# Kernel tuning notes

Hardware: AMD Instinct MI355X
Metric: run time of the kernel (lower is better)

Reference implementation:

```python
import jax, jax.numpy as jnp
import numpy as np
from jax import lax

PAD_ID = 50256
POOL = 2  # maxout pool size


def setup_inputs() -> dict:
    key = jax.random.key(0)
    ks = jax.random.split(key, 20)
    B, T, S = 32, 64, 400
    V, DW, DM, DE, DK = 50257, 512, 512, 512, 64
    s = 0.02
    return {
        "tgt_seq": jax.random.randint(ks[0], (B, T), 0, V, dtype=jnp.int32),
        "src_seq": jax.random.randint(ks[1], (B, S), 0, V, dtype=jnp.int32),
        "enc_output": jax.random.normal(ks[2], (B, S, DE), dtype=jnp.float32),
        "hidden": jax.random.normal(ks[3], (B, DE), dtype=jnp.float32),
        "word_emb": jax.random.normal(ks[4], (V, DW), dtype=jnp.float32) * s,
        "W_init": jax.random.normal(ks[5], (DE, DM), dtype=jnp.float32) * s,
        "b_init": jnp.zeros((DM,), jnp.float32),
        "Wx": jax.random.normal(ks[6], (DW + DE, 3 * DM), dtype=jnp.float32) * s,
        "Wh": jax.random.normal(ks[7], (DM, 3 * DM), dtype=jnp.float32) * s,
        "bx": jnp.zeros((3 * DM,), jnp.float32),
        "bh": jnp.zeros((3 * DM,), jnp.float32),
        "Wc": jax.random.normal(ks[8], (DE, DK), dtype=jnp.float32) * s,
        "Wq": jax.random.normal(ks[9], (DM, DK), dtype=jnp.float32) * s,
        "w_cov": jax.random.normal(ks[10], (DK,), dtype=jnp.float32) * s,
        "v_att": jax.random.normal(ks[11], (DK,), dtype=jnp.float32) * s,
        "W_copy": jax.random.normal(ks[12], (DE + DM, 1), dtype=jnp.float32) * s,
        "b_copy": jnp.zeros((1,), jnp.float32),
        "W_read": jax.random.normal(ks[13], (DW + DM + DE, DM), dtype=jnp.float32) * s,
        "b_read": jnp.zeros((DM,), jnp.float32),
    }


def _gru_cell(x, h, Wx, Wh, bx, bh):
    gx = x @ Wx + bx
    gh = h @ Wh + bh
    rx, zx, nx = jnp.split(gx, 3, axis=-1)
    rh, zh, nh = jnp.split(gh, 3, axis=-1)
    r = jax.nn.sigmoid(rx + rh)
    z = jax.nn.sigmoid(zx + zh)
    n = jnp.tanh(nx + r * nh)
    return (1.0 - z) * n + z * h


def reference(tgt_seq, src_seq, enc_output, hidden, word_emb, W_init, b_init,
              Wx, Wh, bx, bh, Wc, Wq, w_cov, v_att, W_copy, b_copy, W_read, b_read):
    B, S, DE = enc_output.shape
    T = tgt_seq.shape[1]
    DM = Wh.shape[0]
    dt = enc_output.dtype

    pad_mask = (src_seq == PAD_ID)                       # [B,S]
    h0 = jnp.tanh(hidden @ W_init + b_init)              # DecInit  [B,DM]
    ctx0 = jnp.zeros((B, DE), dt)                        # attn_init
    cov0 = jnp.zeros((B, S), dt)
    precompute = jnp.einsum('bsd,dk->bsk', enc_output, Wc)  # computed once
    emb = jnp.swapaxes(word_emb[tgt_seq], 0, 1)          # [T,B,DW]

    def step(carry, x):
        h, ctx, cov = carry
        e, t = x
        rnn_in = jnp.concatenate([e, ctx], axis=1)       # input feed
        h = _gru_cell(rnn_in, h, Wx, Wh, bx, bh)
        # concat attention with coverage
        energy = jnp.tanh(precompute + (h @ Wq)[:, None, :]
                          + cov[:, :, None] * w_cov)     # [B,S,DK]
        scores = energy @ v_att                          # [B,S]
        scores = jnp.where(pad_mask, jnp.asarray(-1e9, dt), scores)
        attn = jax.nn.softmax(scores, axis=1)
        new_ctx = jnp.einsum('bs,bsd->bd', attn, enc_output)
        avg_cov = cov / jnp.maximum(t, 1).astype(dt)
        cov_loss = jnp.sum(jnp.minimum(attn, avg_cov), axis=1)
        next_cov = cov + attn
        copy_gate = jax.nn.sigmoid(jnp.concatenate([h, new_ctx], 1) @ W_copy + b_copy)
        readout = jnp.concatenate([e, h, new_ctx], 1) @ W_read + b_read
        maxo = readout.reshape(B, DM // POOL, POOL).max(axis=2)
        return (h, new_ctx, next_cov), (maxo, attn, copy_gate, cov_loss)

    (_, ctx_f, _), (pred, attns, gates, cov_losses) = lax.scan(
        step, (h0, ctx0, cov0), (emb, jnp.arange(T)))
    pred = jnp.swapaxes(pred, 0, 1)              # [B,T,DM//POOL]
    copy_pred = jnp.swapaxes(attns, 0, 1)        # [B,T,S]
    copy_gate = jnp.swapaxes(gates, 0, 1)        # [B,T,1]
    coverage_pred = jnp.swapaxes(cov_losses, 0, 1)  # [B,T]
    return (pred, attns[-1], ctx_f, copy_pred, copy_gate, coverage_pred)
```

## Files before the change

kernel.cpp:

```cpp
#include <hip/hip_runtime.h>
#include <cstdint>
#include <cstddef>


#define PAD_ID_C 50256

typedef float f32x4 __attribute__((ext_vector_type(4)));
typedef short bf16x8 __attribute__((ext_vector_type(8)));

__device__ __forceinline__ unsigned short f2bf(float x){
  union { float f; unsigned u; } v; v.f = x;
  unsigned r = (v.u + 0x7FFFu + ((v.u >> 16) & 1u)) >> 16;
  return (unsigned short)r;
}
__device__ __forceinline__ float bf2f(unsigned short h){
  union { unsigned u; float f; } v; v.u = ((unsigned)h) << 16; return v.f;
}
__device__ __forceinline__ float sigm_(float x){ return 1.f/(1.f+__expf(-x)); }
__device__ __forceinline__ float tanh_(float x){ float e=__expf(2.f*x); return 1.f - 2.f/(e+1.f); }

__device__ __forceinline__ void cstf(float* p, float v){
  __hip_atomic_store(p, v, __ATOMIC_RELAXED, __HIP_MEMORY_SCOPE_AGENT);
}
__device__ __forceinline__ void csts(unsigned short* p, unsigned short v){
  __hip_atomic_store(p, v, __ATOMIC_RELAXED, __HIP_MEMORY_SCOPE_AGENT);
}

__device__ __forceinline__ int pkidx(int b, int d){
  return ((((b>>4)*16) + (d>>5))*64 + (((d>>3)&3)*16) + (b&15))*8 + (d&7);
}


__global__ void k_pack(const float* __restrict__ W, unsigned short* __restrict__ pk, int N, int K){
  int ktc = K >> 5;
  int gid = blockIdx.x*256 + threadIdx.x;
  int total = (N>>4)*ktc*64;
  if (gid >= total) return;
  int lane = gid & 63;
  int rem = gid >> 6;
  int kt = rem % ktc, nt = rem / ktc;
  int k0 = kt*32 + (lane>>4)*8;
  int n  = nt*16 + (lane&15);
  #pragma unroll
  for (int j=0;j<8;j++) pk[gid*8+j] = f2bf(W[(k0+j)*N + n]);
}

__global__ void k_misc(const float* __restrict__ Wq, unsigned short* __restrict__ wq_t,
                       int* __restrict__ barz){
  int idx = blockIdx.x*256 + threadIdx.x;
  if (idx < 32768){ int k = idx >> 9, d = idx & 511; wq_t[idx] = f2bf(Wq[d*64+k]); }
  else if (idx < 32768 + 4112) barz[idx - 32768] = 0;
}

__global__ void k_emb(const int* __restrict__ tgt, const float* __restrict__ word_emb,
                      unsigned short* __restrict__ emb_pk){
  int bid = blockIdx.x;
  int t = bid >> 5, b = bid & 31;
  int token = tgt[b*64 + t];
  const float* src = word_emb + (size_t)token*512;
  for (int d = threadIdx.x; d < 512; d += 256){
    int idx = (((t*2 + (b>>4))*16 + (d>>5))*64 + ((d>>3)&3)*16 + (b&15))*8 + (d&7);
    emb_pk[idx] = f2bf(src[d]);
  }
}

__global__ void k_encbf(const float* __restrict__ enc, unsigned short* __restrict__ enc_bf){
  int idx = blockIdx.x*256 + threadIdx.x;
  if (idx < 32*400*512) enc_bf[idx] = f2bf(enc[idx]);
}

__global__ void k_pre(const float* __restrict__ enc, const float* __restrict__ Wc,
                      unsigned short* __restrict__ pre_t){
  __shared__ float part[4][64];
  int bs = blockIdx.x;
  int k = threadIdx.x & 63, dp = threadIdx.x >> 6;
  const float* e = enc + (size_t)bs*512;
  float acc = 0.f;
  for (int d = dp*128; d < dp*128 + 128; d++) acc += e[d]*Wc[d*64+k];
  part[dp][k] = acc;
  __syncthreads();
  if (threadIdx.x < 64){
    float a = part[0][k] + part[1][k] + part[2][k] + part[3][k];
    pre_t[(size_t)bs*64 + k] = f2bf(a);
  }
}

__global__ void k_h0(const float* __restrict__ hidden, const float* __restrict__ W_init,
                     const float* __restrict__ b_init,
                     float* __restrict__ hf0, unsigned short* __restrict__ hpk0,
                     float* __restrict__ cf0, unsigned short* __restrict__ cpk0){
  int b = blockIdx.x, jj = threadIdx.x;
  const float* hv = hidden + b*512;
  float acc = 0.f;
  for (int d=0; d<512; d++) acc += hv[d]*W_init[d*512+jj];
  float h = tanh_(acc + b_init[jj]);
  hf0[b*512+jj] = h;
  hpk0[pkidx(b,jj)] = f2bf(h);
  cf0[b*512+jj] = 0.f;
  cpk0[b*512+jj] = 0;
}

__global__ void k_gxe(const unsigned short* __restrict__ emb_pk,
                      const unsigned short* __restrict__ wxe,
                      const float* __restrict__ bx, const float* __restrict__ bh,
                      float* __restrict__ gxe){
  int job = blockIdx.x*4 + (threadIdx.x>>6);
  int lane = threadIdx.x & 63;
  int nt = job % 96, mtg = job / 96;
  f32x4 acc = {0.f,0.f,0.f,0.f};
  const bf16x8* ae = (const bf16x8*)emb_pk + (size_t)(mtg*16)*64 + lane;
  const bf16x8* wp = (const bf16x8*)wxe + (size_t)(nt*16)*64 + lane;
  #pragma unroll
  for (int kt=0; kt<16; kt++)
    acc = __builtin_amdgcn_mfma_f32_16x16x32_bf16(ae[kt*64], wp[kt*64], acc, 0,0,0);
  int row = mtg*16 + (lane>>4)*4, col = nt*16 + (lane&15);
  float badd = bx[col] + (col < 1024 ? bh[col] : 0.f);
  #pragma unroll
  for (int i=0;i<4;i++) gxe[(size_t)(row+i)*1536 + col] = acc[i] + badd;
}


struct PP {
  const unsigned short *emb, *wxc, *wh, *wr, *wq, *pre, *enc;
  const float *gxe;
  unsigned short *hpk, *cpk;
  float *gb;
  float *hf, *cf;
  const float *Wcopy, *bcopy, *bh, *bread, *wcov, *vatt;
  const int* src;
  float *out_pred, *out_attnlast, *out_ctxf, *out_copypred, *out_gate, *out_covloss;
  int *arr;
};

__device__ __forceinline__ void gridbar(int* arr, int idx){
  asm volatile("s_waitcnt vmcnt(0) lgkmcnt(0)" ::: "memory");
  __syncthreads();
  if (threadIdx.x == 0)
    __hip_atomic_store(arr + blockIdx.x*16, idx, __ATOMIC_RELAXED, __HIP_MEMORY_SCOPE_AGENT);
  if (threadIdx.x < 256){
    while (__hip_atomic_load(arr + threadIdx.x*16, __ATOMIC_RELAXED, __HIP_MEMORY_SCOPE_AGENT) < idx){}
  }
  __syncthreads();
}

__device__ __forceinline__ float blockReduceSum(float v, float* redw, int tid){
  #pragma unroll
  for (int off=32; off; off>>=1) v += __shfl_down(v, off, 64);
  if ((tid & 63) == 0) redw[tid>>6] = v;
  __syncthreads();
  if (tid == 0){
    float r = 0.f;
    #pragma unroll
    for (int i=0;i<8;i++) r += redw[i];
    redw[8] = r;
  }
  __syncthreads();
  return redw[8];
}

__global__ __launch_bounds__(512,1) void k_steps(PP p){
  __shared__ float h_s[512];
  __shared__ float gxe_s[1536];
  __shared__ float hq_part[8][64];
  __shared__ float hq_s[64];
  __shared__ float wv_s[128];
  __shared__ float p_s[400];
  __shared__ float redw[16];
  __shared__ float cred[64][65];

  const int tid = threadIdx.x;
  const int b = blockIdx.x & 31, g = blockIdx.x >> 5;
  int idx = 0;
  float c_reg = 0.f;

  if (tid < 128) wv_s[tid] = (tid < 64) ? p.wcov[tid] : p.vatt[tid-64];
  h_s[tid] = p.hf[b*512 + tid];
  const bool padv = (tid < 400) ? (p.src[b*400+tid] == PAD_ID_C) : true;
  const float bh2r = p.bh[1024 + tid];
  const int sown = tid/50 == g ? 1 : 0;
  bf16x8 wqreg[8];
  {
    int k = tid & 63, pr = tid >> 6;
    const bf16x8* wrow = (const bf16x8*)(p.wq + k*512 + pr*64);
    #pragma unroll
    for (int c=0;c<8;c++) wqreg[c] = wrow[c];
  }
  __syncthreads();

  for (int t = 0; t < 64; ++t){
    const unsigned short* hpk_t = p.hpk + (size_t)t*16384;
    const unsigned short* cpk_t = p.cpk + (size_t)t*16384;
    float* gb_t = p.gb + (size_t)t*65536;

    {
      int wib = tid >> 6, lane = tid & 63;
      if (wib == 0){
        if (blockIdx.x < 192){
          int nt = blockIdx.x % 96, mt = blockIdx.x / 96;
          f32x4 aX = {0.f,0.f,0.f,0.f}, aH = {0.f,0.f,0.f,0.f};
          const bf16x8* wpX = (const bf16x8*)p.wxc + (size_t)(nt*16)*64 + lane;
          const bf16x8* wpH = (const bf16x8*)p.wh  + (size_t)(nt*16)*64 + lane;
          const bf16x8* ac = (const bf16x8*)cpk_t + (size_t)(mt*16)*64 + lane;
          const bf16x8* ah = (const bf16x8*)hpk_t + (size_t)(mt*16)*64 + lane;
          #pragma unroll
          for (int kt=0; kt<16; kt++){
            aX = __builtin_amdgcn_mfma_f32_16x16x32_bf16(ac[kt*64], wpX[kt*64], aX, 0,0,0);
            aH = __builtin_amdgcn_mfma_f32_16x16x32_bf16(ah[kt*64], wpH[kt*64], aH, 0,0,0);
          }
          int row = mt*16 + (lane>>4)*4, col = nt*16 + (lane&15);
          if (col < 1024){
            #pragma unroll
            for (int i=0;i<4;i++) cstf(&gb_t[(row+i)*2048 + col], aX[i]+aH[i]);
          } else {
            #pragma unroll
            for (int i=0;i<4;i++){
              cstf(&gb_t[(row+i)*2048 + col], aX[i]);
              cstf(&gb_t[(row+i)*2048 + col + 512], aH[i]);
            }
          }
        }
      } else {
        const float* gxer = p.gxe + (size_t)((t*2 + (b>>4))*16 + (b&15))*1536;
        for (int i = tid - 64; i < 1536; i += 448) gxe_s[i] = gxer[i];
      }
    }
    gridbar(p.arr, ++idx);

    float* hf_w = p.hf + (size_t)(t+1)*16384;
    unsigned short* hpk_w = p.hpk + (size_t)(t+1)*16384;
    float* cf_w = p.cf + (size_t)(t+1)*16384;
    unsigned short* cpk_w = p.cpk + (size_t)(t+1)*16384;

    {
      int jj = tid;
      const float* gbr = gb_t + b*2048;
      float s0 = gbr[jj], s1 = gbr[512+jj], x2 = gbr[1024+jj], y2 = gbr[1536+jj];
      float e0 = gxe_s[jj], e1 = gxe_s[512+jj], e2 = gxe_s[1024+jj];
      float r = sigm_(e0 + s0);
      float z = sigm_(e1 + s1);
      float n = tanh_(e2 + x2 + r*(y2 + bh2r));
      float hold = h_s[jj];
      float hn = (1.f - z)*n + z*hold;
      __syncthreads();
      h_s[jj] = hn;
      if ((tid>>6) == g){ cstf(&hf_w[b*512+jj], hn); csts(&hpk_w[pkidx(b,jj)], f2bf(hn)); }
    }
    __syncthreads();

    {
      int k = tid & 63, pr = tid >> 6;
      float a = 0.f;
      #pragma unroll
      for (int c=0;c<8;c++){
        #pragma unroll
        for (int j=0;j<8;j++) a += h_s[pr*64 + c*8 + j]*bf2f((unsigned short)wqreg[c][j]);
      }
      hq_part[pr][k] = a;
    }
    __syncthreads();
    if (tid < 64){
      float a = 0.f;
      #pragma unroll
      for (int pr=0;pr<8;pr++) a += hq_part[pr][tid];
      hq_s[tid] = a;
    }
    __syncthreads();

    float c_old = c_reg, p_val = 0.f;
    if (tid < 400){
      const unsigned short* prow = p.pre + ((size_t)b*400 + tid)*64;
      float a = 0.f;
      #pragma unroll
      for (int kk=0; kk<8; kk++){
        bf16x8 v = *(const bf16x8*)(prow + kk*8);
        #pragma unroll
        for (int j=0;j<8;j++){
          int k = kk*8 + j;
          float e = bf2f((unsigned short)v[j]) + hq_s[k] + c_old*wv_s[k];
          a += tanh_(e)*wv_s[64+k];
        }
      }
      p_val = padv ? 0.f : __expf(a);
      p_s[tid] = p_val;
    }
    float total = blockReduceSum((tid < 400) ? p_val : 0.f, redw, tid);
    float inv_total = 1.f/total;

    float cl = 0.f;
    float inv_t = 1.f/(float)(t < 1 ? 1 : t);
    if (tid < 400){
      float attnv = p_val*inv_total;
      if (sown){
        p.out_copypred[((size_t)b*64 + t)*400 + tid] = attnv;
        if (t == 63) p.out_attnlast[b*400+tid] = attnv;
      }
      cl = fminf(attnv, c_old*inv_t);
      c_reg = c_old + attnv;
    }
    float cls = blockReduceSum(cl, redw, tid);
    if (g == 0 && tid == 0) p.out_covloss[b*64 + t] = cls;

    {
      int dv = tid & 7, sp = tid >> 3;
      int dgb = g*64 + dv*8;
      float acc[8] = {0.f,0.f,0.f,0.f,0.f,0.f,0.f,0.f};
      const unsigned short* ebase = p.enc + (size_t)(b*400)*512 + dgb;
      for (int ss = sp; ss < 400; ss += 64){
        bf16x8 v = *(const bf16x8*)(ebase + (size_t)ss*512);
        float pw = p_s[ss];
        #pragma unroll
        for (int j=0;j<8;j++) acc[j] += pw*bf2f((unsigned short)v[j]);
      }
      #pragma unroll
      for (int j=0;j<8;j++) cred[sp][dv*8+j] = acc[j];
    }
    __syncthreads();
    if (tid < 64){
      float cx = 0.f;
      #pragma unroll
      for (int s2=0;s2<64;s2++) cx += cred[s2][tid];
      cx *= inv_total;
      int dg = g*64 + tid;
      cstf(&cf_w[b*512+dg], cx);
      csts(&cpk_w[pkidx(b,dg)], f2bf(cx));
      if (t == 63) p.out_ctxf[b*512+dg] = cx;
    }
    gridbar(p.arr, ++idx);
  }

  {
    int wslot = blockIdx.x*8 + (tid>>6);
    int lane = tid & 63;

    for (int job = wslot; job < 4096; job += 2048){
      int nt = job & 31, mtg = job >> 5;
      int t = mtg >> 1, half = mtg & 1;
      f32x4 acc = {0.f,0.f,0.f,0.f};
      const bf16x8* wp = (const bf16x8*)p.wr + (size_t)(nt*48)*64 + lane;
      const bf16x8* ae = (const bf16x8*)p.emb + (size_t)(mtg*16)*64 + lane;
      const bf16x8* ah = (const bf16x8*)(p.hpk + (size_t)(t+1)*16384) + (size_t)(half*16)*64 + lane;
      const bf16x8* ac = (const bf16x8*)(p.cpk + (size_t)(t+1)*16384) + (size_t)(half*16)*64 + lane;
      #pragma unroll
      for (int kt=0; kt<16; kt++)
        acc = __builtin_amdgcn_mfma_f32_16x16x32_bf16(ae[kt*64], wp[kt*64], acc, 0,0,0);
      #pragma unroll
      for (int kt=0; kt<16; kt++)
        acc = __builtin_amdgcn_mfma_f32_16x16x32_bf16(ah[kt*64], wp[(16+kt)*64], acc, 0,0,0);
      #pragma unroll
      for (int kt=0; kt<16; kt++)
        acc = __builtin_amdgcn_mfma_f32_16x16x32_bf16(ac[kt*64], wp[(32+kt)*64], acc, 0,0,0);
      int colL = nt*16 + (lane&15);
      int b0 = half*16 + (lane>>4)*4;
      #pragma unroll
      for (int i=0;i<4;i++){
        float v = acc[i] + p.bread[colL];
        float o = __shfl_xor(v, 1, 64);
        if (!(lane & 1)){
          p.out_pred[((size_t)(b0+i)*64 + t)*256 + nt*8 + ((lane&15)>>1)] = fmaxf(v, o);
        }
      }
    }

    {
      int b2 = wslot >> 6, t = wslot & 63;
      const float* hfr = p.hf + (size_t)(t+1)*16384 + b2*512;
      const float* cfr = p.cf + (size_t)(t+1)*16384 + b2*512;
      float acc = 0.f;
      #pragma unroll
      for (int i=0;i<16;i++){
        int j = i*64 + lane;
        float x = (j < 512) ? hfr[j] : cfr[j-512];
        acc += x * p.Wcopy[j];
      }
      #pragma unroll
      for (int off=32; off>0; off>>=1) acc += __shfl_down(acc, off, 64);
      if (lane == 0) p.out_gate[b2*64 + t] = sigm_(acc + p.bcopy[0]);
    }
  }
}

extern "C" void kernel_launch(void* const* d_in, const int* in_sizes, int n_in,
                              void* d_out, int out_size, void* d_ws, size_t ws_size,
                              hipStream_t stream) {
  const int*   tgt     = (const int*)  d_in[0];
  const int*   src     = (const int*)  d_in[1];
  const float* enc     = (const float*)d_in[2];
  const float* hidden  = (const float*)d_in[3];
  const float* wemb    = (const float*)d_in[4];
  const float* W_init  = (const float*)d_in[5];
  const float* b_init  = (const float*)d_in[6];
  const float* Wx      = (const float*)d_in[7];
  const float* Wh      = (const float*)d_in[8];
  const float* bx      = (const float*)d_in[9];
  const float* bh      = (const float*)d_in[10];
  const float* Wc      = (const float*)d_in[11];
  const float* Wq      = (const float*)d_in[12];
  const float* w_cov   = (const float*)d_in[13];
  const float* v_att   = (const float*)d_in[14];
  const float* W_copy  = (const float*)d_in[15];
  const float* b_copy  = (const float*)d_in[16];
  const float* W_read  = (const float*)d_in[17];
  const float* b_read  = (const float*)d_in[18];

  float* out0 = (float*)d_out;
  float* out1 = out0 + 524288;
  float* out2 = out0 + 537088;
  float* out3 = out0 + 553472;
  float* out4 = out0 + 1372672;
  float* out5 = out0 + 1374720;

  uint8_t* w = (uint8_t*)d_ws;
  unsigned short* emb_pk = (unsigned short*)(w);
  unsigned short* enc_bf = (unsigned short*)(w + 2097152);
  unsigned short* pre_t  = (unsigned short*)(w + 15204352);
  unsigned short* wxe_pk = (unsigned short*)(w + 16842752);
  unsigned short* wxc_pk = (unsigned short*)(w + 18415616);
  unsigned short* wh_pk  = (unsigned short*)(w + 19988480);
  unsigned short* wr_pk  = (unsigned short*)(w + 21561344);
  unsigned short* wq_t   = (unsigned short*)(w + 23134208);
  float* gxe    = (float*)(w + 23199744);
  float* gb_sl  = (float*)(w + 35782656);
  unsigned short* hpk_sl = (unsigned short*)(w + 52559872);
  unsigned short* cpk_sl = (unsigned short*)(w + 54689792);
  float* hf_sl  = (float*)(w + 56819712);
  float* cf_sl  = (float*)(w + 61079552);
  int*   arr    = (int*)  (w + 65339392);

  k_pack<<<384, 256, 0, stream>>>(Wx, wxe_pk, 1536, 512);
  k_pack<<<384, 256, 0, stream>>>(Wx + (size_t)512*1536, wxc_pk, 1536, 512);
  k_pack<<<384, 256, 0, stream>>>(Wh, wh_pk, 1536, 512);
  k_pack<<<384, 256, 0, stream>>>(W_read, wr_pk, 512, 1536);
  k_misc<<<145, 256, 0, stream>>>(Wq, wq_t, arr);
  k_emb<<<2048, 256, 0, stream>>>(tgt, wemb, emb_pk);
  k_encbf<<<25600, 256, 0, stream>>>(enc, enc_bf);
  k_pre<<<12800, 256, 0, stream>>>(enc, Wc, pre_t);
  k_h0<<<32, 512, 0, stream>>>(hidden, W_init, b_init, hf_sl, hpk_sl, cf_sl, cpk_sl);
  k_gxe<<<3072, 256, 0, stream>>>(emb_pk, wxe_pk, bx, bh, gxe);

  PP p;
  p.emb = emb_pk; p.wxc = wxc_pk; p.wh = wh_pk; p.wr = wr_pk; p.wq = wq_t;
  p.pre = pre_t; p.enc = enc_bf; p.gxe = gxe;
  p.hpk = hpk_sl; p.cpk = cpk_sl;
  p.gb = gb_sl;
  p.hf = hf_sl; p.cf = cf_sl;
  p.Wcopy = W_copy; p.bcopy = b_copy; p.bh = bh; p.bread = b_read;
  p.wcov = w_cov; p.vatt = v_att; p.src = src;
  p.out_pred = out0; p.out_attnlast = out1; p.out_ctxf = out2;
  p.out_copypred = out3; p.out_gate = out4; p.out_covloss = out5;
  p.arr = arr;

  void* kargs[] = { (void*)&p };
  hipLaunchCooperativeKernel((const void*)k_steps, dim3(256), dim3(512), kargs, 0, stream);
}
```

Measured before the change: 1.689 ms.

## Run recurrent steps on 32 blocks with narrower grid barrier; fuse enc bf16 conversion

The recurrent loop now runs on 32 blocks, one per batch row, instead of 256 blocks that split the context reduction over groups. The grid barrier only polls those 32 blocks. The other 224 blocks sleep-wait until the recurrence finishes and then join the readout phase. Each active block now does six MFMA gate tiles per step and the whole 512-wide context reduction itself, which cuts the cost of the grid barrier but puts more work on each block. The enc-to-bf16 conversion is also folded into k_pre, which removes one kernel launch and a second full read of enc.

```diff
diff --git a/kernel.cpp b/kernel.cpp
--- a/kernel.cpp
+++ b/kernel.cpp
@@ -64,20 +64,22 @@
   }
 }
 
-__global__ void k_encbf(const float* __restrict__ enc, unsigned short* __restrict__ enc_bf){
-  int idx = blockIdx.x*256 + threadIdx.x;
-  if (idx < 32*400*512) enc_bf[idx] = f2bf(enc[idx]);
-}
-
 __global__ void k_pre(const float* __restrict__ enc, const float* __restrict__ Wc,
-                      unsigned short* __restrict__ pre_t){
+                      unsigned short* __restrict__ pre_t,
+                      unsigned short* __restrict__ enc_bf){
   __shared__ float part[4][64];
   int bs = blockIdx.x;
   int k = threadIdx.x & 63, dp = threadIdx.x >> 6;
   const float* e = enc + (size_t)bs*512;
   float acc = 0.f;
+  #pragma unroll 4
   for (int d = dp*128; d < dp*128 + 128; d++) acc += e[d]*Wc[d*64+k];
   part[dp][k] = acc;
+  {
+    int d0 = dp*128 + k*2;
+    enc_bf[(size_t)bs*512 + d0]     = f2bf(e[d0]);
+    enc_bf[(size_t)bs*512 + d0 + 1] = f2bf(e[d0+1]);
+  }
   __syncthreads();
   if (threadIdx.x < 64){
     float a = part[0][k] + part[1][k] + part[2][k] + part[3][k];
@@ -132,12 +134,12 @@
   int *arr;
 };
 
-__device__ __forceinline__ void gridbar(int* arr, int idx){
+__device__ __forceinline__ void gridbar32(int* arr, int idx){
   asm volatile("s_waitcnt vmcnt(0) lgkmcnt(0)" ::: "memory");
   __syncthreads();
   if (threadIdx.x == 0)
     __hip_atomic_store(arr + blockIdx.x*16, idx, __ATOMIC_RELAXED, __HIP_MEMORY_SCOPE_AGENT);
-  if (threadIdx.x < 256){
+  if (threadIdx.x < 32){
     while (__hip_atomic_load(arr + threadIdx.x*16, __ATOMIC_RELAXED, __HIP_MEMORY_SCOPE_AGENT) < idx){}
   }
   __syncthreads();
@@ -166,37 +168,44 @@
   __shared__ float wv_s[128];
   __shared__ float p_s[400];
   __shared__ float redw[16];
-  __shared__ float cred[64][65];
+  __shared__ float cred[8][512];
 
   const int tid = threadIdx.x;
-  const int b = blockIdx.x & 31, g = blockIdx.x >> 5;
-  int idx = 0;
-  float c_reg = 0.f;
-
-  if (tid < 128) wv_s[tid] = (tid < 64) ? p.wcov[tid] : p.vatt[tid-64];
-  h_s[tid] = p.hf[b*512 + tid];
-  const bool padv = (tid < 400) ? (p.src[b*400+tid] == PAD_ID_C) : true;
-  const float bh2r = p.bh[1024 + tid];
-  const int sown = tid/50 == g ? 1 : 0;
-  bf16x8 wqreg[8];
-  {
-    int k = tid & 63, pr = tid >> 6;
-    const bf16x8* wrow = (const bf16x8*)(p.wq + k*512 + pr*64);
-    #pragma unroll
-    for (int c=0;c<8;c++) wqreg[c] = wrow[c];
-  }
-  __syncthreads();
-
-  for (int t = 0; t < 64; ++t){
-    const unsigned short* hpk_t = p.hpk + (size_t)t*16384;
-    const unsigned short* cpk_t = p.cpk + (size_t)t*16384;
-    float* gb_t = p.gb + (size_t)t*65536;
-
+
+  if (blockIdx.x >= 32){
+    if (tid < 32){
+      while (__hip_atomic_load(p.arr + tid*16, __ATOMIC_RELAXED, __HIP_MEMORY_SCOPE_AGENT) < 128)
+        __builtin_amdgcn_s_sleep(16);
+    }
+    __syncthreads();
+  } else {
+    const int b = blockIdx.x;
+    int idx = 0;
+    float c_reg = 0.f;
+
+    if (tid < 128) wv_s[tid] = (tid < 64) ? p.wcov[tid] : p.vatt[tid-64];
+    h_s[tid] = p.hf[b*512 + tid];
+    const bool padv = (tid < 400) ? (p.src[b*400+tid] == PAD_ID_C) : true;
+    const float bh2r = p.bh[1024 + tid];
+    bf16x8 wqreg[8];
     {
-      int wib = tid >> 6, lane = tid & 63;
-      if (wib == 0){
-        if (blockIdx.x < 192){
-          int nt = blockIdx.x % 96, mt = blockIdx.x / 96;
+      int k = tid & 63, pr = tid >> 6;
+      const bf16x8* wrow = (const bf16x8*)(p.wq + k*512 + pr*64);
+      #pragma unroll
+      for (int c=0;c<8;c++) wqreg[c] = wrow[c];
+    }
+    __syncthreads();
+
+    for (int t = 0; t < 64; ++t){
+      const unsigned short* hpk_t = p.hpk + (size_t)t*16384;
+      const unsigned short* cpk_t = p.cpk + (size_t)t*16384;
+      float* gb_t = p.gb + (size_t)t*65536;
+
+      {
+        int wib = tid >> 6, lane = tid & 63;
+        if (wib < 6){
+          int wv = wib*32 + blockIdx.x;
+          int nt = wv % 96, mt = wv / 96;
           f32x4 aX = {0.f,0.f,0.f,0.f}, aH = {0.f,0.f,0.f,0.f};
           const bf16x8* wpX = (const bf16x8*)p.wxc + (size_t)(nt*16)*64 + lane;
           const bf16x8* wpH = (const bf16x8*)p.wh  + (size_t)(nt*16)*64 + lane;
@@ -218,114 +227,111 @@
               cstf(&gb_t[(row+i)*2048 + col + 512], aH[i]);
             }
           }
+        } else {
+          const float* gxer = p.gxe + (size_t)((t*2 + (b>>4))*16 + (b&15))*1536;
+          for (int i = tid - 384; i < 1536; i += 128) gxe_s[i] = gxer[i];
         }
-      } else {
-        const float* gxer = p.gxe + (size_t)((t*2 + (b>>4))*16 + (b&15))*1536;
-        for (int i = tid - 64; i < 1536; i += 448) gxe_s[i] = gxer[i];
-      }
-    }
-    gridbar(p.arr, ++idx);
-
-    float* hf_w = p.hf + (size_t)(t+1)*16384;
-    unsigned short* hpk_w = p.hpk + (size_t)(t+1)*16384;
-    float* cf_w = p.cf + (size_t)(t+1)*16384;
-    unsigned short* cpk_w = p.cpk + (size_t)(t+1)*16384;
-
-    {
-      int jj = tid;
-      const float* gbr = gb_t + b*2048;
-      float s0 = gbr[jj], s1 = gbr[512+jj], x2 = gbr[1024+jj], y2 = gbr[1536+jj];
-      float e0 = gxe_s[jj], e1 = gxe_s[512+jj], e2 = gxe_s[1024+jj];
-      float r = sigm_(e0 + s0);
-      float z = sigm_(e1 + s1);
-      float n = tanh_(e2 + x2 + r*(y2 + bh2r));
-      float hold = h_s[jj];
-      float hn = (1.f - z)*n + z*hold;
+      }
+      gridbar32(p.arr, ++idx);
+
+      float* hf_w = p.hf + (size_t)(t+1)*16384;
+      unsigned short* hpk_w = p.hpk + (size_t)(t+1)*16384;
+      float* cf_w = p.cf + (size_t)(t+1)*16384;
+      unsigned short* cpk_w = p.cpk + (size_t)(t+1)*16384;
+
+      {
+        int jj = tid;
+        const float* gbr = gb_t + b*2048;
+        float s0 = gbr[jj], s1 = gbr[512+jj], x2 = gbr[1024+jj], y2 = gbr[1536+jj];
+        float e0 = gxe_s[jj], e1 = gxe_s[512+jj], e2 = gxe_s[1024+jj];
+        float r = sigm_(e0 + s0);
+        float z = sigm_(e1 + s1);
+        float n = tanh_(e2 + x2 + r*(y2 + bh2r));
+        float hold = h_s[jj];
+        float hn = (1.f - z)*n + z*hold;
+        __syncthreads();
+        h_s[jj] = hn;
+        cstf(&hf_w[b*512+jj], hn); csts(&hpk_w[pkidx(b,jj)], f2bf(hn));
+      }
       __syncthreads();
-      h_s[jj] = hn;
-      if ((tid>>6) == g){ cstf(&hf_w[b*512+jj], hn); csts(&hpk_w[pkidx(b,jj)], f2bf(hn)); }
-    }
-    __syncthreads();
-
-    {
-      int k = tid & 63, pr = tid >> 6;
-      float a = 0.f;
-      #pragma unroll
-      for (int c=0;c<8;c++){
+
+      {
+        int k = tid & 63, pr = tid >> 6;
+        float a = 0.f;
         #pragma unroll
-        for (int j=0;j<8;j++) a += h_s[pr*64 + c*8 + j]*bf2f((unsigned short)wqreg[c][j]);
-      }
-      hq_part[pr][k] = a;
-    }
-    __syncthreads();
-    if (tid < 64){
-      float a = 0.f;
-      #pragma unroll
-      for (int pr=0;pr<8;pr++) a += hq_part[pr][tid];
-      hq_s[tid] = a;
-    }
-    __syncthreads();
-
-    float c_old = c_reg, p_val = 0.f;
-    if (tid < 400){
-      const unsigned short* prow = p.pre + ((size_t)b*400 + tid)*64;
-      float a = 0.f;
-      #pragma unroll
-      for (int kk=0; kk<8; kk++){
-        bf16x8 v = *(const bf16x8*)(prow + kk*8);
+        for (int c=0;c<8;c++){
+          #pragma unroll
+          for (int j=0;j<8;j++) a += h_s[pr*64 + c*8 + j]*bf2f((unsigned short)wqreg[c][j]);
+        }
+        hq_part[pr][k] = a;
+      }
+      __syncthreads();
+      if (tid < 64){
+        float a = 0.f;
         #pragma unroll
-        for (int j=0;j<8;j++){
-          int k = kk*8 + j;
-          float e = bf2f((unsigned short)v[j]) + hq_s[k] + c_old*wv_s[k];
-          a += tanh_(e)*wv_s[64+k];
+        for (int pr=0;pr<8;pr++) a += hq_part[pr][tid];
+        hq_s[tid] = a;
+      }
+      __syncthreads();
+
+      float c_old = c_reg, p_val = 0.f;
+      if (tid < 400){
+        const unsigned short* prow = p.pre + ((size_t)b*400 + tid)*64;
+        float a = 0.f;
+        #pragma unroll
+        for (int kk=0; kk<8; kk++){
+          bf16x8 v = *(const bf16x8*)(prow + kk*8);
+          #pragma unroll
+          for (int j=0;j<8;j++){
+            int k = kk*8 + j;
+            float e = bf2f((unsigned short)v[j]) + hq_s[k] + c_old*wv_s[k];
+            a += tanh_(e)*wv_s[64+k];
+          }
         }
-      }
-      p_val = padv ? 0.f : __expf(a);
-      p_s[tid] = p_val;
-    }
-    float total = blockReduceSum((tid < 400) ? p_val : 0.f, redw, tid);
-    float inv_total = 1.f/total;
-
-    float cl = 0.f;
-    float inv_t = 1.f/(float)(t < 1 ? 1 : t);
-    if (tid < 400){
-      float attnv = p_val*inv_total;
-      if (sown){
+        p_val = padv ? 0.f : __expf(a);
+        p_s[tid] = p_val;
+      }
+      float total = blockReduceSum((tid < 400) ? p_val : 0.f, redw, tid);
+      float inv_total = 1.f/total;
+
+      float cl = 0.f;
+      float inv_t = 1.f/(float)(t < 1 ? 1 : t);
+      if (tid < 400){
+        float attnv = p_val*inv_total;
         p.out_copypred[((size_t)b*64 + t)*400 + tid] = attnv;
         if (t == 63) p.out_attnlast[b*400+tid] = attnv;
-      }
-      cl = fminf(attnv, c_old*inv_t);
-      c_reg = c_old + attnv;
+        cl = fminf(attnv, c_old*inv_t);
+        c_reg = c_old + attnv;
+      }
+      float cls = blockReduceSum(cl, redw, tid);
+      if (tid == 0) p.out_covloss[b*64 + t] = cls;
+
+      {
+        int wib = tid >> 6, lane = tid & 63;
+        float acc[8] = {0.f,0.f,0.f,0.f,0.f,0.f,0.f,0.f};
+        const unsigned short* ebase = p.enc + (size_t)(b*400)*512 + lane*8;
+        #pragma unroll 2
+        for (int ss = wib*50; ss < wib*50 + 50; ++ss){
+          bf16x8 v = *(const bf16x8*)(ebase + (size_t)ss*512);
+          float pw = p_s[ss];
+          #pragma unroll
+          for (int j=0;j<8;j++) acc[j] += pw*bf2f((unsigned short)v[j]);
+        }
+        #pragma unroll
+        for (int j=0;j<8;j++) cred[wib][lane*8+j] = acc[j];
+      }
+      __syncthreads();
+      {
+        float cx = 0.f;
+        #pragma unroll
+        for (int w2=0;w2<8;w2++) cx += cred[w2][tid];
+        cx *= inv_total;
+        cstf(&cf_w[b*512+tid], cx);
+        csts(&cpk_w[pkidx(b,tid)], f2bf(cx));
+        if (t == 63) p.out_ctxf[b*512+tid] = cx;
+      }
+      gridbar32(p.arr, ++idx);
     }
-    float cls = blockReduceSum(cl, redw, tid);
-    if (g == 0 && tid == 0) p.out_covloss[b*64 + t] = cls;
-
-    {
-      int dv = tid & 7, sp = tid >> 3;
-      int dgb = g*64 + dv*8;
-      float acc[8] = {0.f,0.f,0.f,0.f,0.f,0.f,0.f,0.f};
-      const unsigned short* ebase = p.enc + (size_t)(b*400)*512 + dgb;
-      for (int ss = sp; ss < 400; ss += 64){
-        bf16x8 v = *(const bf16x8*)(ebase + (size_t)ss*512);
-        float pw = p_s[ss];
-        #pragma unroll
-        for (int j=0;j<8;j++) acc[j] += pw*bf2f((unsigned short)v[j]);
-      }
-      #pragma unroll
-      for (int j=0;j<8;j++) cred[sp][dv*8+j] = acc[j];
-    }
-    __syncthreads();
-    if (tid < 64){
-      float cx = 0.f;
-      #pragma unroll
-      for (int s2=0;s2<64;s2++) cx += cred[s2][tid];
-      cx *= inv_total;
-      int dg = g*64 + tid;
-      cstf(&cf_w[b*512+dg], cx);
-      csts(&cpk_w[pkidx(b,dg)], f2bf(cx));
-      if (t == 63) p.out_ctxf[b*512+dg] = cx;
-    }
-    gridbar(p.arr, ++idx);
   }
 
   {
@@ -432,8 +438,7 @@
   k_pack<<<384, 256, 0, stream>>>(W_read, wr_pk, 512, 1536);
   k_misc<<<145, 256, 0, stream>>>(Wq, wq_t, arr);
   k_emb<<<2048, 256, 0, stream>>>(tgt, wemb, emb_pk);
-  k_encbf<<<25600, 256, 0, stream>>>(enc, enc_bf);
-  k_pre<<<12800, 256, 0, stream>>>(enc, Wc, pre_t);
+  k_pre<<<12800, 256, 0, stream>>>(enc, Wc, pre_t, enc_bf);
   k_h0<<<32, 512, 0, stream>>>(hidden, W_init, b_init, hf_sl, hpk_sl, cf_sl, cpk_sl);
   k_gxe<<<3072, 256, 0, stream>>>(emb_pk, wxe_pk, bx, bh, gxe);
 
```

New measurement: 1.769 ms. 4.8% more time.
